# Optimization experiments

Hardware: AMD Instinct MI355X
Metric: run time of the kernel (lower is better)

Reference implementation:

```python
import jax, jax.numpy as jnp
import numpy as np

N = 100000      # num_nodes
E = 1600000     # num_edges
T = 6           # num_time_steps
F_IN = 64       # num_features (must equal hidden=64, see notes)
HID = 64
C_OUT = 16      # num_classes
C = 0.1         # curvature c


def setup_inputs() -> dict:
    key = jax.random.key(0)
    ks = jax.random.split(key, 7)
    x = jax.random.normal(ks[0], (N, F_IN), dtype=jnp.float32)
    edge_index = jax.random.randint(ks[1], (2, E), 0, N, dtype=jnp.int32)
    time_index = jax.random.randint(ks[2], (E,), 0, T, dtype=jnp.int32)
    # temporal_lin weights, stored as [in, out] (torch nn.Linear is [out, in])
    s1 = 1.0 / np.sqrt(T * HID)
    W1 = jax.random.uniform(ks[3], (T * HID, HID), jnp.float32, -s1, s1)
    b1 = jax.random.uniform(ks[4], (HID,), jnp.float32, -s1, s1)
    W2 = jax.random.uniform(ks[5], (T * HID, C_OUT), jnp.float32, -s1, s1)
    b2 = jax.random.uniform(ks[6], (C_OUT,), jnp.float32, -s1, s1)
    return {"x": x, "edge_index": edge_index, "time_index": time_index,
            "W1": W1, "b1": b1, "W2": W2, "b2": b2}


def hyperbolic_conv(x, src, dst, time_index, W, b, c, num_time_steps):
    # Fused per-timestep scatter: segment id = t * N + dst gives one combined
    # segment_sum instead of T masked passes over the edge list.
    n, f = x.shape
    x_src = x[src]                                   # [E, F] gather
    seg = time_index.astype(jnp.int32) * n + dst     # [E]
    sums = jax.ops.segment_sum(x_src, seg, num_segments=num_time_steps * n)  # [T*N, F]
    cnt = jax.ops.segment_sum(jnp.ones_like(src, dtype=x.dtype), seg,
                              num_segments=num_time_steps * n)               # [T*N]
    mean = sums / jnp.clip(cnt, 1.0)[:, None]        # [T*N, F]
    # hyperbolic normalization: mean / (1 - c^2 * ||mean||^2)
    norm_mean = 1.0 - (c * c) * jnp.sum(mean * mean, axis=-1, keepdims=True)
    h = mean / norm_mean                              # [T*N, F]
    # torch.cat(temporal_outputs, dim=-1): [N, T*F], t-major in feature dim
    h = h.reshape(num_time_steps, n, f).transpose(1, 0, 2).reshape(n, num_time_steps * f)
    return jax.nn.relu(h @ W + b)


def reference(x, edge_index, time_index, W1, b1, W2, b2):
    src, dst = edge_index[0], edge_index[1]
    h = hyperbolic_conv(x, src, dst, time_index, W1, b1, C, T)   # [N, 64]
    h = jax.nn.relu(h)                                           # outer relu in model.forward
    out = hyperbolic_conv(h, src, dst, time_index, W2, b2, C, T) # [N, 16]
    return out
```

## Files before the change

kernel.cpp:

```cpp
#include <hip/hip_runtime.h>

#define N_NODES 100000
#define N_PAD   100032
#define N_EDGES 1600000
#define T_STEPS 6
#define FDIM    64
#define SEG     (T_STEPS * N_NODES)
#define C2      0.01f
#define PADF    68
#define RFL __builtin_amdgcn_readfirstlane

__global__ __launch_bounds__(256) void k_build(
    const int* __restrict__ src, const int* __restrict__ dst,
    const int* __restrict__ tix, int* __restrict__ head,
    int2* __restrict__ edat)
{
  const int e = blockIdx.x * blockDim.x + threadIdx.x;
  if (e >= N_EDGES) return;
  const int key = tix[e] * N_NODES + dst[e];
  const int prev = atomicExch(&head[key], e);
  edat[e] = make_int2(src[e], prev);
}

__global__ __launch_bounds__(256) void k_sum6(
    const float* __restrict__ feat, const int2* __restrict__ edat,
    const int* __restrict__ head, float* __restrict__ sums,
    float* __restrict__ cnt)
{
  const int lane = threadIdx.x & 63;
  const int n = blockIdx.x * (blockDim.x >> 6) + (threadIdx.x >> 6);
  if (n >= N_NODES) return;

  int e0 = RFL(head[(size_t)0 * N_NODES + n]);
  int e1 = RFL(head[(size_t)1 * N_NODES + n]);
  int e2 = RFL(head[(size_t)2 * N_NODES + n]);
  int e3 = RFL(head[(size_t)3 * N_NODES + n]);
  int e4 = RFL(head[(size_t)4 * N_NODES + n]);
  int e5 = RFL(head[(size_t)5 * N_NODES + n]);

  float v0 = 0.f, v1 = 0.f, v2 = 0.f, v3 = 0.f, v4 = 0.f, v5 = 0.f;
  int c0 = 0, c1 = 0, c2 = 0, c3 = 0, c4 = 0, c5 = 0;

  while ((e0 >= 0) | (e1 >= 0) | (e2 >= 0) | (e3 >= 0) | (e4 >= 0) | (e5 >= 0)) {
    const int a0 = e0 < 0 ? 0 : e0, a1 = e1 < 0 ? 0 : e1, a2 = e2 < 0 ? 0 : e2;
    const int a3 = e3 < 0 ? 0 : e3, a4 = e4 < 0 ? 0 : e4, a5 = e5 < 0 ? 0 : e5;

    const int2 d0 = edat[a0];
    const int2 d1 = edat[a1];
    const int2 d2 = edat[a2];
    const int2 d3 = edat[a3];
    const int2 d4 = edat[a4];
    const int2 d5 = edat[a5];

    const int s0 = RFL(d0.x), x0 = RFL(d0.y);
    const int s1 = RFL(d1.x), x1 = RFL(d1.y);
    const int s2 = RFL(d2.x), x2 = RFL(d2.y);
    const int s3 = RFL(d3.x), x3 = RFL(d3.y);
    const int s4 = RFL(d4.x), x4 = RFL(d4.y);
    const int s5 = RFL(d5.x), x5 = RFL(d5.y);

    const float f0 = feat[(size_t)s0 * FDIM + lane];
    const float f1 = feat[(size_t)s1 * FDIM + lane];
    const float f2 = feat[(size_t)s2 * FDIM + lane];
    const float f3 = feat[(size_t)s3 * FDIM + lane];
    const float f4 = feat[(size_t)s4 * FDIM + lane];
    const float f5 = feat[(size_t)s5 * FDIM + lane];

    v0 += (e0 >= 0) ? f0 : 0.0f;  c0 += (e0 >= 0);  e0 = (e0 >= 0) ? x0 : -1;
    v1 += (e1 >= 0) ? f1 : 0.0f;  c1 += (e1 >= 0);  e1 = (e1 >= 0) ? x1 : -1;
    v2 += (e2 >= 0) ? f2 : 0.0f;  c2 += (e2 >= 0);  e2 = (e2 >= 0) ? x2 : -1;
    v3 += (e3 >= 0) ? f3 : 0.0f;  c3 += (e3 >= 0);  e3 = (e3 >= 0) ? x3 : -1;
    v4 += (e4 >= 0) ? f4 : 0.0f;  c4 += (e4 >= 0);  e4 = (e4 >= 0) ? x4 : -1;
    v5 += (e5 >= 0) ? f5 : 0.0f;  c5 += (e5 >= 0);  e5 = (e5 >= 0) ? x5 : -1;
  }

  sums[((size_t)0 * N_PAD + n) * FDIM + lane] = v0;
  sums[((size_t)1 * N_PAD + n) * FDIM + lane] = v1;
  sums[((size_t)2 * N_PAD + n) * FDIM + lane] = v2;
  sums[((size_t)3 * N_PAD + n) * FDIM + lane] = v3;
  sums[((size_t)4 * N_PAD + n) * FDIM + lane] = v4;
  sums[((size_t)5 * N_PAD + n) * FDIM + lane] = v5;
  if (lane == 0) {
    cnt[(size_t)0 * N_NODES + n] = (float)c0;
    cnt[(size_t)1 * N_NODES + n] = (float)c1;
    cnt[(size_t)2 * N_NODES + n] = (float)c2;
    cnt[(size_t)3 * N_NODES + n] = (float)c3;
    cnt[(size_t)4 * N_NODES + n] = (float)c4;
    cnt[(size_t)5 * N_NODES + n] = (float)c5;
  }
}

template <int OUTF, int JBLK>
__global__ __launch_bounds__(256) void k_gemm_tile2(
    const float* __restrict__ sums, const float* __restrict__ cnt,
    const float* __restrict__ W, const float* __restrict__ bias,
    float* __restrict__ out)
{
  __shared__ float lds[2][64 * PADF];
  const int tid = threadIdx.x;
  const int lane = tid & 63;
  const int n0 = blockIdx.x * 64;
  const int jb = RFL(tid >> 6) * JBLK;

  int n = n0 + lane;
  const bool valid = (n < N_NODES);
  if (!valid) n = N_NODES - 1;

  float acc[JBLK];
  #pragma unroll
  for (int j = 0; j < JBLK; ++j) acc[j] = bias[jb + j];

  #pragma unroll 1
  for (int tp = 0; tp < T_STEPS / 2; ++tp) {
    __syncthreads();
    float4 reg[8];
    #pragma unroll
    for (int it = 0; it < 8; ++it) {
      const int item = tid + it * 256;
      const int q = item & 15;
      const int u = (item >> 4) & 63;
      const int pl = item >> 10;
      reg[it] = *(const float4*)(sums + ((size_t)(2 * tp + pl) * N_PAD + n0 + u) * FDIM + q * 4);
    }
    #pragma unroll
    for (int it = 0; it < 8; ++it) {
      const int item = tid + it * 256;
      const int q = item & 15;
      const int u = (item >> 4) & 63;
      const int pl = item >> 10;
      *(float4*)(&lds[pl][u * PADF + q * 4]) = reg[it];
    }
    __syncthreads();

    #pragma unroll
    for (int pl = 0; pl < 2; ++pl) {
      const int t = 2 * tp + pl;

      const float c  = cnt[(size_t)t * N_NODES + n];
      const float rc = 1.0f / fmaxf(c, 1.0f);
      const float4* row = (const float4*)(&lds[pl][lane * PADF]);
      float ss = 0.0f;
      #pragma unroll
      for (int q = 0; q < FDIM / 4; ++q) {
        float4 v = row[q];
        float m0 = v.x * rc, m1 = v.y * rc, m2 = v.z * rc, m3 = v.w * rc;
        ss += m0 * m0 + m1 * m1 + m2 * m2 + m3 * m3;
      }
      const float norm = 1.0f - C2 * ss;
      const float s = rc / norm;

      #pragma unroll
      for (int q8 = 0; q8 < FDIM / 8; ++q8) {
        const float4 a = row[q8 * 2 + 0];
        const float4 b4 = row[q8 * 2 + 1];
        const float hv[8] = {a.x, a.y, a.z, a.w, b4.x, b4.y, b4.z, b4.w};
        const float* wr = W + ((size_t)t * FDIM + q8 * 8) * OUTF + jb;
        #pragma unroll
        for (int i = 0; i < 8; ++i) {
          const float hs = hv[i] * s;
          #pragma unroll
          for (int j = 0; j < JBLK; ++j)
            acc[j] = fmaf(hs, wr[i * OUTF + j], acc[j]);
        }
      }
    }
  }

  if (valid) {
    float* o = out + (size_t)n * OUTF + jb;
    #pragma unroll
    for (int j = 0; j < JBLK; ++j) o[j] = fmaxf(acc[j], 0.0f);
  }
}

extern "C" void kernel_launch(void* const* d_in, const int* in_sizes, int n_in,
                              void* d_out, int out_size, void* d_ws, size_t ws_size,
                              hipStream_t stream) {
  const float* x  = (const float*)d_in[0];
  const int*  ei  = (const int*)d_in[1];
  const int*  tix = (const int*)d_in[2];
  const float* W1 = (const float*)d_in[3];
  const float* b1 = (const float*)d_in[4];
  const float* W2 = (const float*)d_in[5];
  const float* b2 = (const float*)d_in[6];

  const int* src = ei;
  const int* dst = ei + N_EDGES;

  int*   head = (int*)d_ws;
  int2*  edat = (int2*)(head + SEG);
  float* sums = (float*)(edat + N_EDGES);
  float* cnt  = sums + (size_t)T_STEPS * N_PAD * FDIM;
  float* h1   = cnt + SEG;

  const int sum_grid = (N_NODES + 3) / 4;
  const int ngrp     = (N_NODES + 63) / 64;

  hipMemsetAsync(head, 0xFF, (size_t)SEG * sizeof(int), stream);
  k_build<<<(N_EDGES + 255) / 256, 256, 0, stream>>>(src, dst, tix, head, edat);

  k_sum6<<<sum_grid, 256, 0, stream>>>(x, edat, head, sums, cnt);
  k_gemm_tile2<64, 16><<<ngrp, 256, 0, stream>>>(sums, cnt, W1, b1, h1);

  k_sum6<<<sum_grid, 256, 0, stream>>>(h1, edat, head, sums, cnt);
  k_gemm_tile2<16, 4><<<ngrp, 256, 0, stream>>>(sums, cnt, W2, b2, (float*)d_out);
}
```

Measured before the change: 424.9 us.

## Stage GEMM input tiles via global_load_lds with double-buffered per-timestep prefetch

```diff
diff --git a/kernel.cpp b/kernel.cpp
--- a/kernel.cpp
+++ b/kernel.cpp
@@ -90,8 +90,14 @@
   }
 }
 
+__device__ __forceinline__ void gl16(const float* g, float* l) {
+  __builtin_amdgcn_global_load_lds(
+      (const __attribute__((address_space(1))) void*)g,
+      (__attribute__((address_space(3))) void*)l, 16, 0, 0);
+}
+
 template <int OUTF, int JBLK>
-__global__ __launch_bounds__(256) void k_gemm_tile2(
+__global__ __launch_bounds__(256) void k_gemm_gl(
     const float* __restrict__ sums, const float* __restrict__ cnt,
     const float* __restrict__ W, const float* __restrict__ bias,
     float* __restrict__ out)
@@ -99,8 +105,9 @@
   __shared__ float lds[2][64 * PADF];
   const int tid = threadIdx.x;
   const int lane = tid & 63;
+  const int wv = RFL(tid >> 6);
   const int n0 = blockIdx.x * 64;
-  const int jb = RFL(tid >> 6) * JBLK;
+  const int jb = wv * JBLK;
 
   int n = n0 + lane;
   const bool valid = (n < N_NODES);
@@ -110,61 +117,54 @@
   #pragma unroll
   for (int j = 0; j < JBLK; ++j) acc[j] = bias[jb + j];
 
+  #define STAGE_PL(B, T)                                                      \
+    for (int c = wv; c < 17; c += 4) {                                        \
+      const int p  = c * 64 + lane;                \
+      const int u  = p / 17;                                   \
+      const int qq = (p % 17) & 15;        \
+      gl16(sums + ((size_t)(T) * N_PAD + n0 + u) * FDIM + qq * 4,             \
+           &lds[B][0] + c * 256);                                             \
+    }
+
+  STAGE_PL(0, 0);
+  __syncthreads();
+
   #pragma unroll 1
-  for (int tp = 0; tp < T_STEPS / 2; ++tp) {
-    __syncthreads();
-    float4 reg[8];
+  for (int t = 0; t < T_STEPS; ++t) {
+    const float* row4 = &lds[t & 1][lane * PADF];
+    if (t + 1 < T_STEPS) { STAGE_PL((t + 1) & 1, t + 1); }
+
+    const float c  = cnt[(size_t)t * N_NODES + n];
+    const float rc = 1.0f / fmaxf(c, 1.0f);
+    const float4* row = (const float4*)row4;
+    float ss = 0.0f;
     #pragma unroll
-    for (int it = 0; it < 8; ++it) {
-      const int item = tid + it * 256;
-      const int q = item & 15;
-      const int u = (item >> 4) & 63;
-      const int pl = item >> 10;
-      reg[it] = *(const float4*)(sums + ((size_t)(2 * tp + pl) * N_PAD + n0 + u) * FDIM + q * 4);
+    for (int q = 0; q < FDIM / 4; ++q) {
+      float4 v = row[q];
+      float m0 = v.x * rc, m1 = v.y * rc, m2 = v.z * rc, m3 = v.w * rc;
+      ss += m0 * m0 + m1 * m1 + m2 * m2 + m3 * m3;
     }
+    const float norm = 1.0f - C2 * ss;
+    const float s = rc / norm;
+
     #pragma unroll
-    for (int it = 0; it < 8; ++it) {
-      const int item = tid + it * 256;
-      const int q = item & 15;
-      const int u = (item >> 4) & 63;
-      const int pl = item >> 10;
-      *(float4*)(&lds[pl][u * PADF + q * 4]) = reg[it];
-    }
-    __syncthreads();
-
-    #pragma unroll
-    for (int pl = 0; pl < 2; ++pl) {
-      const int t = 2 * tp + pl;
-
-      const float c  = cnt[(size_t)t * N_NODES + n];
-      const float rc = 1.0f / fmaxf(c, 1.0f);
-      const float4* row = (const float4*)(&lds[pl][lane * PADF]);
-      float ss = 0.0f;
+    for (int q8 = 0; q8 < FDIM / 8; ++q8) {
+      const float4 a = row[q8 * 2 + 0];
+      const float4 b4 = row[q8 * 2 + 1];
+      const float hv[8] = {a.x, a.y, a.z, a.w, b4.x, b4.y, b4.z, b4.w};
+      const float* wr = W + ((size_t)t * FDIM + q8 * 8) * OUTF + jb;
       #pragma unroll
-      for (int q = 0; q < FDIM / 4; ++q) {
-        float4 v = row[q];
-        float m0 = v.x * rc, m1 = v.y * rc, m2 = v.z * rc, m3 = v.w * rc;
-        ss += m0 * m0 + m1 * m1 + m2 * m2 + m3 * m3;
-      }
-      const float norm = 1.0f - C2 * ss;
-      const float s = rc / norm;
-
-      #pragma unroll
-      for (int q8 = 0; q8 < FDIM / 8; ++q8) {
-        const float4 a = row[q8 * 2 + 0];
-        const float4 b4 = row[q8 * 2 + 1];
-        const float hv[8] = {a.x, a.y, a.z, a.w, b4.x, b4.y, b4.z, b4.w};
-        const float* wr = W + ((size_t)t * FDIM + q8 * 8) * OUTF + jb;
+      for (int i = 0; i < 8; ++i) {
+        const float hs = hv[i] * s;
         #pragma unroll
-        for (int i = 0; i < 8; ++i) {
-          const float hs = hv[i] * s;
-          #pragma unroll
-          for (int j = 0; j < JBLK; ++j)
-            acc[j] = fmaf(hs, wr[i * OUTF + j], acc[j]);
-        }
+        for (int j = 0; j < JBLK; ++j)
+          acc[j] = fmaf(hs, wr[i * OUTF + j], acc[j]);
       }
     }
-  }
+
+    __syncthreads();
+  }
+  #undef STAGE_PL
 
   if (valid) {
     float* o = out + (size_t)n * OUTF + jb;
@@ -200,8 +200,8 @@
   k_build<<<(N_EDGES + 255) / 256, 256, 0, stream>>>(src, dst, tix, head, edat);
 
   k_sum6<<<sum_grid, 256, 0, stream>>>(x, edat, head, sums, cnt);
-  k_gemm_tile2<64, 16><<<ngrp, 256, 0, stream>>>(sums, cnt, W1, b1, h1);
+  k_gemm_gl<64, 16><<<ngrp, 256, 0, stream>>>(sums, cnt, W1, b1, h1);
 
   k_sum6<<<sum_grid, 256, 0, stream>>>(h1, edat, head, sums, cnt);
-  k_gemm_tile2<16, 4><<<ngrp, 256, 0, stream>>>(sums, cnt, W2, b2, (float*)d_out);
-}
+  k_gemm_gl<16, 4><<<ngrp, 256, 0, stream>>>(sums, cnt, W2, b2, (float*)d_out);
+}
```

Measured after the change: 425.4 us. No clear change (+0.1%).
